# Kernel tuning notes

Hardware: AMD Instinct MI355X
Metric: run time of the kernel (lower is better)

## Reference

```python
import jax, jax.numpy as jnp
import numpy as np

N = 50000
E = 800000
IN_C = 128
HID = 64
HEADS = 4
OUT_C = 64
NEG_SLOPE = 0.2


def gat_conv(x, edge_index, W, att_src, att_dst, bias, heads, out_ch, concat):
    """PyG-style GATConv (add_self_loops=True, eval mode: no dropout)."""
    n = x.shape[0]
    loop = jnp.arange(n, dtype=edge_index.dtype)
    src = jnp.concatenate([edge_index[0], loop])
    dst = jnp.concatenate([edge_index[1], loop])
    h = (x @ W).reshape(n, heads, out_ch)              # [N,H,C]
    a_s = jnp.einsum('nhc,hc->nh', h, att_src)          # [N,H]
    a_d = jnp.einsum('nhc,hc->nh', h, att_dst)
    e = jax.nn.leaky_relu(a_s[src] + a_d[dst], NEG_SLOPE)  # [E',H]
    m = jax.ops.segment_max(e, dst, num_segments=n)
    m = jnp.where(jnp.isfinite(m), m, 0.0)
    ex = jnp.exp(e - m[dst])
    denom = jax.ops.segment_sum(ex, dst, num_segments=n)
    alpha = ex / (denom[dst] + 1e-16)                   # segment softmax over incoming edges
    out = jax.ops.segment_sum(alpha[:, :, None] * h[src], dst, num_segments=n)  # [N,H,C]
    out = out.reshape(n, heads * out_ch) if concat else out.mean(axis=1)
    return out + bias


def setup_inputs() -> dict:
    key = jax.random.key(0)
    ks = jax.random.split(key, 20)
    s = 0.1
    inp = {
        'x': jax.random.normal(ks[0], (N, IN_C), dtype=jnp.float32),
        'pos_edge_index': jax.random.randint(ks[1], (2, E), 0, N, dtype=jnp.int32),
        'neg_edge_index': jax.random.randint(ks[2], (2, E), 0, N, dtype=jnp.int32),
        # layer 0 pos
        'W0p': jax.random.normal(ks[3], (IN_C, HEADS * HID), jnp.float32) * s,
        'asrc0p': jax.random.normal(ks[4], (HEADS, HID), jnp.float32) * s,
        'adst0p': jax.random.normal(ks[5], (HEADS, HID), jnp.float32) * s,
        'b0p': jnp.zeros((HEADS * HID,), jnp.float32),
        # layer 0 neg
        'W0n': jax.random.normal(ks[6], (IN_C, HEADS * HID), jnp.float32) * s,
        'asrc0n': jax.random.normal(ks[7], (HEADS, HID), jnp.float32) * s,
        'adst0n': jax.random.normal(ks[8], (HEADS, HID), jnp.float32) * s,
        'b0n': jnp.zeros((HEADS * HID,), jnp.float32),
        # layer 1 pos (heads=1, concat=False)
        'W1p': jax.random.normal(ks[9], (HEADS * HID, OUT_C), jnp.float32) * s,
        'asrc1p': jax.random.normal(ks[10], (1, OUT_C), jnp.float32) * s,
        'adst1p': jax.random.normal(ks[11], (1, OUT_C), jnp.float32) * s,
        'b1p': jnp.zeros((OUT_C,), jnp.float32),
        # layer 1 neg
        'W1n': jax.random.normal(ks[12], (HEADS * HID, OUT_C), jnp.float32) * s,
        'asrc1n': jax.random.normal(ks[13], (1, OUT_C), jnp.float32) * s,
        'adst1n': jax.random.normal(ks[14], (1, OUT_C), jnp.float32) * s,
        'b1n': jnp.zeros((OUT_C,), jnp.float32),
    }
    return inp


def reference(x, pos_edge_index, neg_edge_index,
              W0p, asrc0p, adst0p, b0p,
              W0n, asrc0n, adst0n, b0n,
              W1p, asrc1p, adst1p, b1p,
              W1n, asrc1n, adst1n, b1n):
    xp = gat_conv(x, pos_edge_index, W0p, asrc0p, adst0p, b0p, HEADS, HID, True)
    xn = gat_conv(x, neg_edge_index, W0n, asrc0n, adst0n, b0n, HEADS, HID, True)
    h = jax.nn.elu(xp - xn)  # dropout is identity in eval mode
    op = gat_conv(h, pos_edge_index, W1p, asrc1p, adst1p, b1p, 1, OUT_C, False)
    on = gat_conv(h, neg_edge_index, W1n, asrc1n, adst1n, b1n, 1, OUT_C, False)
    return op - on
```

## Files before the change

### kernel.cpp

```cpp
#include <hip/hip_runtime.h>
#include <cstdint>

#define N_NODES 50000
#define N_EDGES 800000

typedef __attribute__((ext_vector_type(8))) short bf16x8;
typedef __attribute__((ext_vector_type(4))) float f32x4;

__device__ __forceinline__ float lrelu(float x) { return x >= 0.f ? x : 0.2f * x; }

__device__ __forceinline__ void onup(float& m, float& s, float e) {
  float nm = fmaxf(m, e);
  s = s * __expf(m - nm) + __expf(e - nm);
  m = nm;
}

__device__ __forceinline__ unsigned short f2b(float f) {
  unsigned int u = __float_as_uint(f);
  u += 0x7FFFu + ((u >> 16) & 1u);
  return (unsigned short)(u >> 16);
}
__device__ __forceinline__ float blo(unsigned int u) { return __uint_as_float(u << 16); }
__device__ __forceinline__ float bhi(unsigned int u) { return __uint_as_float(u & 0xFFFF0000u); }

__device__ __forceinline__ float sel4(float v0, float v1, float v2, float v3, int h) {
  float r = v0;
  r = (h == 1) ? v1 : r;
  r = (h == 2) ? v2 : r;
  r = (h == 3) ? v3 : r;
  return r;
}


__global__ __launch_bounds__(256) void k_hist2(const int* __restrict__ ep, const int* __restrict__ en,
                                               int* __restrict__ cntP, int* __restrict__ cntN, int E, int half) {
  int b = blockIdx.x;
  const int* ei = (b < half) ? ep : en;
  int* cnt = (b < half) ? cntP : cntN;
  int e = (b % half) * 256 + threadIdx.x;
  if (e < E) atomicAdd(&cnt[ei[E + e]], 1);
}

__global__ __launch_bounds__(256) void k_scan_partial2(const int* __restrict__ cntP, const int* __restrict__ cntN,
                                                       int* __restrict__ partP, int* __restrict__ partN,
                                                       int N, int half) {
  int b = blockIdx.x;
  const int* cnt = (b < half) ? cntP : cntN;
  int* partial = (b < half) ? partP : partN;
  int bb = b % half;
  int t = threadIdx.x;
  int sum = 0;
#pragma unroll
  for (int i = 0; i < 4; i++) {
    int idx = bb * 1024 + i * 256 + t;
    if (idx < N) sum += cnt[idx];
  }
#pragma unroll
  for (int o = 32; o; o >>= 1) sum += __shfl_xor(sum, o);
  __shared__ int sh[4];
  if ((t & 63) == 0) sh[t >> 6] = sum;
  __syncthreads();
  if (t == 0) partial[bb] = sh[0] + sh[1] + sh[2] + sh[3];
}

__global__ __launch_bounds__(64) void k_scan_top2(const int* __restrict__ partP, const int* __restrict__ partN,
                                                  int* __restrict__ prefP, int* __restrict__ prefN,
                                                  int nb, int* __restrict__ offPN, int* __restrict__ offNN, int total) {
  const int* partial = (blockIdx.x == 0) ? partP : partN;
  int* pref = (blockIdx.x == 0) ? prefP : prefN;
  int* offN = (blockIdx.x == 0) ? offPN : offNN;
  int l = threadIdx.x;
  int v = (l < nb) ? partial[l] : 0;
  int x = v;
#pragma unroll
  for (int o = 1; o < 64; o <<= 1) {
    int y = __shfl_up(x, o);
    if (l >= o) x += y;
  }
  if (l < nb) pref[l] = x - v;
  if (l == 0) *offN = total;
}

__global__ __launch_bounds__(256) void k_scan_final2(const int* __restrict__ cntP, const int* __restrict__ cntN,
                                                     const int* __restrict__ prefP, const int* __restrict__ prefN,
                                                     int* __restrict__ offP, int* __restrict__ offN,
                                                     int N, int half) {
  int b = blockIdx.x;
  const int* cnt = (b < half) ? cntP : cntN;
  const int* pref = (b < half) ? prefP : prefN;
  int* off = (b < half) ? offP : offN;
  int bb = b % half;
  int t = threadIdx.x;
  int idx0 = bb * 1024 + t * 4;
  int v0 = (idx0 + 0 < N) ? cnt[idx0 + 0] : 0;
  int v1 = (idx0 + 1 < N) ? cnt[idx0 + 1] : 0;
  int v2 = (idx0 + 2 < N) ? cnt[idx0 + 2] : 0;
  int v3 = (idx0 + 3 < N) ? cnt[idx0 + 3] : 0;
  int s = v0 + v1 + v2 + v3;
  int lane = t & 63, w = t >> 6;
  int x = s;
#pragma unroll
  for (int o = 1; o < 64; o <<= 1) {
    int y = __shfl_up(x, o);
    if (lane >= o) x += y;
  }
  __shared__ int wtot[4];
  if (lane == 63) wtot[w] = x;
  __syncthreads();
  int woff = 0;
#pragma unroll
  for (int i = 0; i < 4; i++)
    if (i < w) woff += wtot[i];
  int excl = pref[bb] + woff + (x - s);
  if (idx0 + 0 < N) off[idx0 + 0] = excl;
  excl += v0;
  if (idx0 + 1 < N) off[idx0 + 1] = excl;
  excl += v1;
  if (idx0 + 2 < N) off[idx0 + 2] = excl;
  excl += v2;
  if (idx0 + 3 < N) off[idx0 + 3] = excl;
}

__global__ __launch_bounds__(256) void k_scatter2(const int* __restrict__ ep, const int* __restrict__ en,
                                                  const int* __restrict__ offP, const int* __restrict__ offN,
                                                  int* __restrict__ cntP, int* __restrict__ cntN,
                                                  int* __restrict__ srtP, int* __restrict__ srtN, int E, int half) {
  int b = blockIdx.x;
  const int* ei = (b < half) ? ep : en;
  const int* off = (b < half) ? offP : offN;
  int* cnt = (b < half) ? cntP : cntN;
  int* srt = (b < half) ? srtP : srtN;
  int e = (b % half) * 256 + threadIdx.x;
  if (e < E) {
    int s = ei[e], d = ei[E + e];
    int p = atomicSub(&cnt[d], 1) - 1;
    srt[off[d] + p] = s;
  }
}


__global__ __launch_bounds__(256) void k_prep(const float* __restrict__ x,
                                              const float* __restrict__ W0p, const float* __restrict__ W0n,
                                              const float* __restrict__ W1p, const float* __restrict__ W1n,
                                              unsigned short* __restrict__ xb,
                                              unsigned short* __restrict__ w0f,
                                              unsigned short* __restrict__ w1f) {
  int b = blockIdx.x, t = threadIdx.x;
  if (b < 3125) {
    int base = (b * 256 + t) * 8;
    float4 v0 = *(const float4*)&x[base];
    float4 v1 = *(const float4*)&x[base + 4];
    ushort4 a, c;
    a.x = f2b(v0.x); a.y = f2b(v0.y); a.z = f2b(v0.z); a.w = f2b(v0.w);
    c.x = f2b(v1.x); c.y = f2b(v1.y); c.z = f2b(v1.z); c.w = f2b(v1.w);
    *(ushort4*)&xb[base] = a;
    *(ushort4*)&xb[base + 4] = c;
  } else if (b < 3157) {
    int tid = (b - 3125) * 256 + t;
    int lane = tid & 63;
    int rest = tid >> 6;
    int ks = rest & 3; rest >>= 2;
    int n = rest & 3;
    int g = rest >> 2;
    int col = (g & 3) * 64 + n * 16 + (lane & 15);
    const float* W = (g < 4) ? W0p : W0n;
    size_t dst = ((((size_t)(g * 4 + n)) * 4 + ks) * 64 + lane) * 8;
#pragma unroll
    for (int j = 0; j < 8; j++) {
      int k = ks * 32 + (lane >> 4) * 8 + j;
      w0f[dst + j] = f2b(W[k * 256 + col]);
    }
  } else {
    int tid = (b - 3157) * 256 + t;
    int lane = tid & 63;
    int rest = tid >> 6;
    int ks = rest & 7; rest >>= 3;
    int n = rest & 3;
    int g = rest >> 2;
    int col = n * 16 + (lane & 15);
    const float* W = g ? W1n : W1p;
    size_t dst = ((((size_t)(g * 4 + n)) * 8 + ks) * 64 + lane) * 8;
#pragma unroll
    for (int j = 0; j < 8; j++) {
      int k = ks * 32 + (lane >> 4) * 8 + j;
      w1f[dst + j] = f2b(W[k * 64 + col]);
    }
  }
}


template <int KSTEPS, int CBF16, int H, int NC>
__global__ __launch_bounds__(256) void k_mgemm(const unsigned short* __restrict__ Ab,
                                               const unsigned short* __restrict__ Bf,
                                               unsigned short* __restrict__ Cb, float* __restrict__ Cf,
                                               int Nrows,
                                               const float* __restrict__ attSP, const float* __restrict__ attDP,
                                               const float* __restrict__ attSN, const float* __restrict__ attDN,
                                               float* __restrict__ oSP, float* __restrict__ oDP,
                                               float* __restrict__ oSN, float* __restrict__ oDN) {
  constexpr int K = KSTEPS * 32;
  int wm = threadIdx.x >> 6, lane = threadIdx.x & 63;
  int row0 = blockIdx.x * 128 + wm * 32;
  int g = blockIdx.y;
  const bf16x8* Bv = (const bf16x8*)Bf;
  const bf16x8* Av = (const bf16x8*)Ab;

  f32x4 acc[2][4];
#pragma unroll
  for (int mi = 0; mi < 2; mi++)
#pragma unroll
    for (int n = 0; n < 4; n++) acc[mi][n] = (f32x4){0.f, 0.f, 0.f, 0.f};

  int r0 = row0 + (lane & 15);
  int r1 = r0 + 16;
  bool v0 = r0 < Nrows, v1 = r1 < Nrows;
  size_t arow0 = (size_t)r0 * (K / 8) + (lane >> 4);
  size_t arow1 = (size_t)r1 * (K / 8) + (lane >> 4);
  const bf16x8 az = {0, 0, 0, 0, 0, 0, 0, 0};

  for (int kh = 0; kh < KSTEPS / 4; kh++) {
#pragma unroll
    for (int k4 = 0; k4 < 4; k4++) {
      int ks = kh * 4 + k4;
      bf16x8 a0 = v0 ? Av[arow0 + ks * 4] : az;
      bf16x8 a1 = v1 ? Av[arow1 + ks * 4] : az;
      bf16x8 b0 = Bv[((size_t)(g * 4 + 0) * KSTEPS + ks) * 64 + lane];
      bf16x8 b1 = Bv[((size_t)(g * 4 + 1) * KSTEPS + ks) * 64 + lane];
      bf16x8 b2 = Bv[((size_t)(g * 4 + 2) * KSTEPS + ks) * 64 + lane];
      bf16x8 b3 = Bv[((size_t)(g * 4 + 3) * KSTEPS + ks) * 64 + lane];
      acc[0][0] = __builtin_amdgcn_mfma_f32_16x16x32_bf16(a0, b0, acc[0][0], 0, 0, 0);
      acc[0][1] = __builtin_amdgcn_mfma_f32_16x16x32_bf16(a0, b1, acc[0][1], 0, 0, 0);
      acc[0][2] = __builtin_amdgcn_mfma_f32_16x16x32_bf16(a0, b2, acc[0][2], 0, 0, 0);
      acc[0][3] = __builtin_amdgcn_mfma_f32_16x16x32_bf16(a0, b3, acc[0][3], 0, 0, 0);
      acc[1][0] = __builtin_amdgcn_mfma_f32_16x16x32_bf16(a1, b0, acc[1][0], 0, 0, 0);
      acc[1][1] = __builtin_amdgcn_mfma_f32_16x16x32_bf16(a1, b1, acc[1][1], 0, 0, 0);
      acc[1][2] = __builtin_amdgcn_mfma_f32_16x16x32_bf16(a1, b2, acc[1][2], 0, 0, 0);
      acc[1][3] = __builtin_amdgcn_mfma_f32_16x16x32_bf16(a1, b3, acc[1][3], 0, 0, 0);
    }
  }

#pragma unroll
  for (int mi = 0; mi < 2; mi++)
#pragma unroll
    for (int n = 0; n < 4; n++)
#pragma unroll
      for (int reg = 0; reg < 4; reg++) {
        int row = row0 + mi * 16 + (lane >> 4) * 4 + reg;
        int col = g * 64 + n * 16 + (lane & 15);
        if (row < Nrows) {
          if (CBF16)
            Cb[(size_t)row * NC + col] = f2b(acc[mi][n][reg]);
          else
            Cf[(size_t)row * NC + col] = acc[mi][n][reg];
        }
      }

  constexpr int POSG = NC / 128;
  int isNeg = (g >= POSG) ? 1 : 0;
  int head = isNeg ? g - POSG : g;
  const float* wS = (isNeg ? attSN : attSP) + head * 64;
  const float* wD = (isNeg ? attDN : attDP) + head * 64;
  float* oS = isNeg ? oSN : oSP;
  float* oD = isNeg ? oDN : oDP;
  float ws0 = wS[0 * 16 + (lane & 15)], ws1 = wS[1 * 16 + (lane & 15)];
  float ws2 = wS[2 * 16 + (lane & 15)], ws3 = wS[3 * 16 + (lane & 15)];
  float wd0 = wD[0 * 16 + (lane & 15)], wd1 = wD[1 * 16 + (lane & 15)];
  float wd2 = wD[2 * 16 + (lane & 15)], wd3 = wD[3 * 16 + (lane & 15)];
#pragma unroll
  for (int mi = 0; mi < 2; mi++)
#pragma unroll
    for (int reg = 0; reg < 4; reg++) {
      float ps = acc[mi][0][reg] * ws0 + acc[mi][1][reg] * ws1 + acc[mi][2][reg] * ws2 + acc[mi][3][reg] * ws3;
      float pd = acc[mi][0][reg] * wd0 + acc[mi][1][reg] * wd1 + acc[mi][2][reg] * wd2 + acc[mi][3][reg] * wd3;
#pragma unroll
      for (int o = 1; o < 16; o <<= 1) {
        ps += __shfl_xor(ps, o);
        pd += __shfl_xor(pd, o);
      }
      int row = row0 + mi * 16 + (lane >> 4) * 4 + reg;
      if ((lane & 15) == 0 && row < Nrows) {
        oS[(size_t)row * H + head] = ps;
        oD[(size_t)row * H + head] = pd;
      }
    }
}


struct MS4 { float m0, m1, m2, m3, s0, s1, s2, s3; };

__device__ __forceinline__ MS4 stats_heads(const float* __restrict__ as, float4 sl, float4 ad,
                                           const int* __restrict__ srt, int base, int deg, int l) {
  MS4 r;
  r.m0 = r.m1 = r.m2 = r.m3 = -1e30f;
  r.s0 = r.s1 = r.s2 = r.s3 = 0.f;
  if (l == 0) {
    r.m0 = lrelu(sl.x + ad.x); r.s0 = 1.f;
    r.m1 = lrelu(sl.y + ad.y); r.s1 = 1.f;
    r.m2 = lrelu(sl.z + ad.z); r.s2 = 1.f;
    r.m3 = lrelu(sl.w + ad.w); r.s3 = 1.f;
  }
  for (int i = l; i < deg; i += 64) {
    int s = srt[base + i];
    float4 av = *(const float4*)&as[(size_t)s * 4];
    onup(r.m0, r.s0, lrelu(av.x + ad.x));
    onup(r.m1, r.s1, lrelu(av.y + ad.y));
    onup(r.m2, r.s2, lrelu(av.z + ad.z));
    onup(r.m3, r.s3, lrelu(av.w + ad.w));
  }
#pragma unroll
  for (int o = 32; o; o >>= 1) {
    float mo, so, nm;
    mo = __shfl_xor(r.m0, o); so = __shfl_xor(r.s0, o);
    nm = fmaxf(r.m0, mo); r.s0 = r.s0 * __expf(r.m0 - nm) + so * __expf(mo - nm); r.m0 = nm;
    mo = __shfl_xor(r.m1, o); so = __shfl_xor(r.s1, o);
    nm = fmaxf(r.m1, mo); r.s1 = r.s1 * __expf(r.m1 - nm) + so * __expf(mo - nm); r.m1 = nm;
    mo = __shfl_xor(r.m2, o); so = __shfl_xor(r.s2, o);
    nm = fmaxf(r.m2, mo); r.s2 = r.s2 * __expf(r.m2 - nm) + so * __expf(mo - nm); r.m2 = nm;
    mo = __shfl_xor(r.m3, o); so = __shfl_xor(r.s3, o);
    nm = fmaxf(r.m3, mo); r.s3 = r.s3 * __expf(r.m3 - nm) + so * __expf(mo - nm); r.m3 = nm;
  }
  return r;
}


__device__ __forceinline__ float4 gather0b(const unsigned short* __restrict__ h0b, int colElem,
                                           const float* __restrict__ as, int hl, float adh,
                                           float mh, float inv, float wself, int n,
                                           const int* __restrict__ srt, int base, int deg, int l) {
  float4 acc;
  {
    uint2 hv = *(const uint2*)&h0b[(size_t)n * 512 + colElem];
    acc.x = wself * blo(hv.x); acc.y = wself * bhi(hv.x);
    acc.z = wself * blo(hv.y); acc.w = wself * bhi(hv.y);
  }
  for (int j = 0; j < deg; j += 8) {
    int idx[8];
    float w[8];
#pragma unroll
    for (int s2 = 0; s2 < 8; s2++) {
      int jj = j + s2;
      bool v = jj < deg;
      int p = base + (v ? jj : 0);
      int si = srt[p];
      idx[s2] = si;
      float e = lrelu(as[(size_t)si * 4 + hl] + adh);
      w[s2] = v ? __expf(e - mh) * inv : 0.f;
    }
#pragma unroll
    for (int s2 = 0; s2 < 8; s2++) {
      uint2 hv = *(const uint2*)&h0b[(size_t)idx[s2] * 512 + colElem];
      acc.x = fmaf(w[s2], blo(hv.x), acc.x);
      acc.y = fmaf(w[s2], bhi(hv.x), acc.y);
      acc.z = fmaf(w[s2], blo(hv.y), acc.z);
      acc.w = fmaf(w[s2], bhi(hv.y), acc.w);
    }
  }
  return acc;
}

__global__ __launch_bounds__(256) void k_agg0f(const unsigned short* __restrict__ h0b,
                                               const float* __restrict__ asP, const float* __restrict__ adP,
                                               const float* __restrict__ asN, const float* __restrict__ adN,
                                               const int* __restrict__ offP, const int* __restrict__ srtP,
                                               const int* __restrict__ offN, const int* __restrict__ srtN,
                                               const float* __restrict__ bP, const float* __restrict__ bN,
                                               unsigned short* __restrict__ xb, int N) {
  int n = blockIdx.x * 4 + (threadIdx.x >> 6);
  if (n >= N) return;
  int l = threadIdx.x & 63;
  int hl = l >> 4;

  int baseP = offP[n], degP = offP[n + 1] - baseP;
  float4 adp4 = *(const float4*)&adP[(size_t)n * 4];
  float4 asp4 = *(const float4*)&asP[(size_t)n * 4];
  MS4 P = stats_heads(asP, asp4, adp4, srtP, baseP, degP, l);
  float mhP = sel4(P.m0, P.m1, P.m2, P.m3, hl);
  float invP = 1.f / (sel4(P.s0, P.s1, P.s2, P.s3, hl) + 1e-16f);
  float adhP = sel4(adp4.x, adp4.y, adp4.z, adp4.w, hl);
  float ashP = sel4(asp4.x, asp4.y, asp4.z, asp4.w, hl);
  float wselfP = __expf(lrelu(ashP + adhP) - mhP) * invP;
  float4 accP = gather0b(h0b, l * 4, asP, hl, adhP, mhP, invP, wselfP, n, srtP, baseP, degP, l);

  int baseN = offN[n], degN = offN[n + 1] - baseN;
  float4 adn4 = *(const float4*)&adN[(size_t)n * 4];
  float4 asn4 = *(const float4*)&asN[(size_t)n * 4];
  MS4 Q = stats_heads(asN, asn4, adn4, srtN, baseN, degN, l);
  float mhN = sel4(Q.m0, Q.m1, Q.m2, Q.m3, hl);
  float invN = 1.f / (sel4(Q.s0, Q.s1, Q.s2, Q.s3, hl) + 1e-16f);
  float adhN = sel4(adn4.x, adn4.y, adn4.z, adn4.w, hl);
  float ashN = sel4(asn4.x, asn4.y, asn4.z, asn4.w, hl);
  float wselfN = __expf(lrelu(ashN + adhN) - mhN) * invN;
  float4 accN = gather0b(h0b, 256 + l * 4, asN, hl, adhN, mhN, invN, wselfN, n, srtN, baseN, degN, l);

  float4 bp = *(const float4*)&bP[l * 4];
  float4 bn = *(const float4*)&bN[l * 4];
  float rx = accP.x + bp.x - accN.x - bn.x;
  float ry = accP.y + bp.y - accN.y - bn.y;
  float rz = accP.z + bp.z - accN.z - bn.z;
  float rw = accP.w + bp.w - accN.w - bn.w;
  rx = rx > 0.f ? rx : expm1f(rx);
  ry = ry > 0.f ? ry : expm1f(ry);
  rz = rz > 0.f ? rz : expm1f(rz);
  rw = rw > 0.f ? rw : expm1f(rw);
  ushort4 r;
  r.x = f2b(rx); r.y = f2b(ry); r.z = f2b(rz); r.w = f2b(rw);
  *(ushort4*)&xb[(size_t)n * 256 + l * 4] = r;
}


__device__ __forceinline__ void stats1(const float* __restrict__ as, float sl, float ad,
                                       const int* __restrict__ srt, int base, int deg, int l,
                                       float& m, float& s) {
  m = -1e30f;
  s = 0.f;
  if (l == 0) {
    m = lrelu(sl + ad);
    s = 1.f;
  }
  for (int i = l; i < deg; i += 64) onup(m, s, lrelu(as[srt[base + i]] + ad));
#pragma unroll
  for (int o = 32; o; o >>= 1) {
    float mo = __shfl_xor(m, o);
    float so = __shfl_xor(s, o);
    float nm = fmaxf(m, mo);
    s = s * __expf(m - nm) + so * __expf(mo - nm);
    m = nm;
  }
}

__device__ __forceinline__ float gather1_half(const float* __restrict__ h1, int colOff,
                                              const float* __restrict__ as, float ad, float mh, float inv,
                                              float wself, int n, const int* __restrict__ srt, int base, int deg,
                                              int l) {
  float acc = wself * h1[(size_t)n * 128 + colOff + l];
  for (int j = 0; j < deg; j += 8) {
    int idx[8];
    float w[8];
#pragma unroll
    for (int s2 = 0; s2 < 8; s2++) {
      int jj = j + s2;
      bool v = jj < deg;
      int p = base + (v ? jj : 0);
      int si = srt[p];
      idx[s2] = si;
      w[s2] = v ? __expf(lrelu(as[si] + ad) - mh) * inv : 0.f;
    }
#pragma unroll
    for (int s2 = 0; s2 < 8; s2++) acc = fmaf(w[s2], h1[(size_t)idx[s2] * 128 + colOff + l], acc);
  }
  return acc;
}

__global__ __launch_bounds__(256) void k_agg1f(const float* __restrict__ h1,
                                               const float* __restrict__ asP, const float* __restrict__ adP,
                                               const float* __restrict__ asN, const float* __restrict__ adN,
                                               const int* __restrict__ offP, const int* __restrict__ srtP,
                                               const int* __restrict__ offN, const int* __restrict__ srtN,
                                               const float* __restrict__ bP, const float* __restrict__ bN,
                                               float* __restrict__ out, int N) {
  int n = blockIdx.x * 4 + (threadIdx.x >> 6);
  if (n >= N) return;
  int l = threadIdx.x & 63;

  int baseP = offP[n], degP = offP[n + 1] - baseP;
  float adp = adP[n], asp = asP[n];
  float mP, sP;
  stats1(asP, asp, adp, srtP, baseP, degP, l, mP, sP);
  float invP = 1.f / (sP + 1e-16f);
  float wselfP = __expf(lrelu(asp + adp) - mP) * invP;
  float accP = gather1_half(h1, 0, asP, adp, mP, invP, wselfP, n, srtP, baseP, degP, l);

  int baseN = offN[n], degN = offN[n + 1] - baseN;
  float adn = adN[n], asn = asN[n];
  float mN, sN;
  stats1(asN, asn, adn, srtN, baseN, degN, l, mN, sN);
  float invN = 1.f / (sN + 1e-16f);
  float wselfN = __expf(lrelu(asn + adn) - mN) * invN;
  float accN = gather1_half(h1, 64, asN, adn, mN, invN, wselfN, n, srtN, baseN, degN, l);

  out[(size_t)n * 64 + l] = (accP + bP[l]) - (accN + bN[l]);
}


extern "C" void kernel_launch(void* const* d_in, const int* in_sizes, int n_in,
                              void* d_out, int out_size, void* d_ws, size_t ws_size,
                              hipStream_t stream) {
  const float* x = (const float*)d_in[0];
  const int* ep = (const int*)d_in[1];
  const int* en = (const int*)d_in[2];
  const float* W0p = (const float*)d_in[3];
  const float* asrc0p = (const float*)d_in[4];
  const float* adst0p = (const float*)d_in[5];
  const float* b0p = (const float*)d_in[6];
  const float* W0n = (const float*)d_in[7];
  const float* asrc0n = (const float*)d_in[8];
  const float* adst0n = (const float*)d_in[9];
  const float* b0n = (const float*)d_in[10];
  const float* W1p = (const float*)d_in[11];
  const float* asrc1p = (const float*)d_in[12];
  const float* adst1p = (const float*)d_in[13];
  const float* b1p = (const float*)d_in[14];
  const float* W1n = (const float*)d_in[15];
  const float* asrc1n = (const float*)d_in[16];
  const float* adst1n = (const float*)d_in[17];
  const float* b1n = (const float*)d_in[18];

  const int N = N_NODES, E = N_EDGES;
  char* base = (char*)d_ws;
  size_t o = 0;
  auto alloc = [&](size_t bytes) -> void* {
    void* r = base + o;
    o = (o + bytes + 255) & ~(size_t)255;
    return r;
  };
  int* cnt_p = (int*)alloc((size_t)N * 4);
  int* cnt_n = (int*)alloc((size_t)N * 4);
  size_t cntBytes = o;
  int* off_p = (int*)alloc((size_t)(N + 1) * 4);
  int* off_n = (int*)alloc((size_t)(N + 1) * 4);
  int* part_p = (int*)alloc(1024 * 4);
  int* part_n = (int*)alloc(1024 * 4);
  int* pref_p = (int*)alloc(1024 * 4);
  int* pref_n = (int*)alloc(1024 * 4);
  int* srt_p = (int*)alloc((size_t)E * 4);
  int* srt_n = (int*)alloc((size_t)E * 4);
  unsigned short* xb16 = (unsigned short*)alloc((size_t)N * 128 * 2);
  unsigned short* w0f = (unsigned short*)alloc(65536 * 2);
  unsigned short* w1f = (unsigned short*)alloc(32768 * 2);
  unsigned short* h0b = (unsigned short*)alloc((size_t)N * 512 * 2);
  float* as0p = (float*)alloc((size_t)N * 4 * 4);
  float* ad0p = (float*)alloc((size_t)N * 4 * 4);
  float* as0n = (float*)alloc((size_t)N * 4 * 4);
  float* ad0n = (float*)alloc((size_t)N * 4 * 4);
  float* as1p = (float*)alloc((size_t)N * 4);
  float* ad1p = (float*)alloc((size_t)N * 4);
  float* as1n = (float*)alloc((size_t)N * 4);
  float* ad1n = (float*)alloc((size_t)N * 4);
  unsigned short* xbufb = (unsigned short*)alloc((size_t)N * 256 * 2);
  float* h1 = (float*)alloc((size_t)N * 128 * 4);

  hipMemsetAsync(base, 0, cntBytes, stream);

  int egrid = (E + 255) / 256;
  int nb = (N + 1023) / 1024;
  k_hist2<<<2 * egrid, 256, 0, stream>>>(ep, en, cnt_p, cnt_n, E, egrid);
  k_scan_partial2<<<2 * nb, 256, 0, stream>>>(cnt_p, cnt_n, part_p, part_n, N, nb);
  k_scan_top2<<<2, 64, 0, stream>>>(part_p, part_n, pref_p, pref_n, nb, off_p + N, off_n + N, E);
  k_scan_final2<<<2 * nb, 256, 0, stream>>>(cnt_p, cnt_n, pref_p, pref_n, off_p, off_n, N, nb);
  k_scatter2<<<2 * egrid, 256, 0, stream>>>(ep, en, off_p, off_n, cnt_p, cnt_n, srt_p, srt_n, E, egrid);

  k_prep<<<3173, 256, 0, stream>>>(x, W0p, W0n, W1p, W1n, xb16, w0f, w1f);

  int ngrid = (N + 3) / 4;
  int mgrid = (N + 127) / 128;

  dim3 g0(mgrid, 8);
  k_mgemm<4, 1, 4, 512><<<g0, 256, 0, stream>>>(xb16, w0f, h0b, (float*)nullptr, N,
                                                asrc0p, adst0p, asrc0n, adst0n,
                                                as0p, ad0p, as0n, ad0n);
  k_agg0f<<<ngrid, 256, 0, stream>>>(h0b, as0p, ad0p, as0n, ad0n,
                                     off_p, srt_p, off_n, srt_n, b0p, b0n, xbufb, N);

  dim3 g1(mgrid, 2);
  k_mgemm<8, 0, 1, 128><<<g1, 256, 0, stream>>>(xbufb, w1f, (unsigned short*)nullptr, h1, N,
                                                asrc1p, adst1p, asrc1n, adst1n,
                                                as1p, ad1p, as1n, ad1n);
  k_agg1f<<<ngrid, 256, 0, stream>>>(h1, as1p, ad1p, as1n, ad1n,
                                     off_p, srt_p, off_n, srt_n, b1p, b1n, (float*)d_out, N);
}
```

Measured before the change: 637.8 us.

## Split attention softmax into separate per-edge exp pass and gather pass

Replaces the fused online-softmax stats plus gather with a separate kernel that computes exp(leaky_relu(e)) per edge without max subtraction, stores it into per-edge alpha buffers, and writes per-node inverse sums and self-loop weights. The gather kernels then read the precomputed alpha and scale by the inverse sum at the end. This avoids recomputing exps and the online max/rescale in the gather. In exchange it adds kernel launches and writes and reads of per-edge alpha arrays. Dropping the max subtraction risks overflow for large logits.

```diff
diff --git a/kernel.cpp b/kernel.cpp
--- a/kernel.cpp
+++ b/kernel.cpp
@@ -8,12 +8,6 @@
 typedef __attribute__((ext_vector_type(4))) float f32x4;
 
 __device__ __forceinline__ float lrelu(float x) { return x >= 0.f ? x : 0.2f * x; }
-
-__device__ __forceinline__ void onup(float& m, float& s, float e) {
-  float nm = fmaxf(m, e);
-  s = s * __expf(m - nm) + __expf(e - nm);
-  m = nm;
-}
 
 __device__ __forceinline__ unsigned short f2b(float f) {
   unsigned int u = __float_as_uint(f);
@@ -22,14 +16,6 @@
 }
 __device__ __forceinline__ float blo(unsigned int u) { return __uint_as_float(u << 16); }
 __device__ __forceinline__ float bhi(unsigned int u) { return __uint_as_float(u & 0xFFFF0000u); }
-
-__device__ __forceinline__ float sel4(float v0, float v1, float v2, float v3, int h) {
-  float r = v0;
-  r = (h == 1) ? v1 : r;
-  r = (h == 2) ? v2 : r;
-  r = (h == 3) ? v3 : r;
-  return r;
-}
 
 
 __global__ __launch_bounds__(256) void k_hist2(const int* __restrict__ ep, const int* __restrict__ en,
@@ -286,53 +272,96 @@
 }
 
 
-struct MS4 { float m0, m1, m2, m3, s0, s1, s2, s3; };
-
-__device__ __forceinline__ MS4 stats_heads(const float* __restrict__ as, float4 sl, float4 ad,
-                                           const int* __restrict__ srt, int base, int deg, int l) {
-  MS4 r;
-  r.m0 = r.m1 = r.m2 = r.m3 = -1e30f;
-  r.s0 = r.s1 = r.s2 = r.s3 = 0.f;
-  if (l == 0) {
-    r.m0 = lrelu(sl.x + ad.x); r.s0 = 1.f;
-    r.m1 = lrelu(sl.y + ad.y); r.s1 = 1.f;
-    r.m2 = lrelu(sl.z + ad.z); r.s2 = 1.f;
-    r.m3 = lrelu(sl.w + ad.w); r.s3 = 1.f;
-  }
-  for (int i = l; i < deg; i += 64) {
-    int s = srt[base + i];
-    float4 av = *(const float4*)&as[(size_t)s * 4];
-    onup(r.m0, r.s0, lrelu(av.x + ad.x));
-    onup(r.m1, r.s1, lrelu(av.y + ad.y));
-    onup(r.m2, r.s2, lrelu(av.z + ad.z));
-    onup(r.m3, r.s3, lrelu(av.w + ad.w));
-  }
-#pragma unroll
-  for (int o = 32; o; o >>= 1) {
-    float mo, so, nm;
-    mo = __shfl_xor(r.m0, o); so = __shfl_xor(r.s0, o);
-    nm = fmaxf(r.m0, mo); r.s0 = r.s0 * __expf(r.m0 - nm) + so * __expf(mo - nm); r.m0 = nm;
-    mo = __shfl_xor(r.m1, o); so = __shfl_xor(r.s1, o);
-    nm = fmaxf(r.m1, mo); r.s1 = r.s1 * __expf(r.m1 - nm) + so * __expf(mo - nm); r.m1 = nm;
-    mo = __shfl_xor(r.m2, o); so = __shfl_xor(r.s2, o);
-    nm = fmaxf(r.m2, mo); r.s2 = r.s2 * __expf(r.m2 - nm) + so * __expf(mo - nm); r.m2 = nm;
-    mo = __shfl_xor(r.m3, o); so = __shfl_xor(r.s3, o);
-    nm = fmaxf(r.m3, mo); r.s3 = r.s3 * __expf(r.m3 - nm) + so * __expf(mo - nm); r.m3 = nm;
-  }
-  return r;
+__global__ __launch_bounds__(256) void k_sa0(const float* __restrict__ asP, const float* __restrict__ adP,
+                                             const int* __restrict__ offP, const int* __restrict__ srtP,
+                                             float* __restrict__ alphaP, float* __restrict__ invP,
+                                             float* __restrict__ wslfP,
+                                             const float* __restrict__ asN, const float* __restrict__ adN,
+                                             const int* __restrict__ offN, const int* __restrict__ srtN,
+                                             float* __restrict__ alphaN, float* __restrict__ invN,
+                                             float* __restrict__ wslfN, int N) {
+  int n = blockIdx.x * 4 + (threadIdx.x >> 6);
+  if (n >= N) return;
+  int l = threadIdx.x & 63;
+  {
+    int base = offP[n], deg = offP[n + 1] - base;
+    float4 ad4 = *(const float4*)&adP[(size_t)n * 4];
+    float s0 = 0.f, s1 = 0.f, s2 = 0.f, s3 = 0.f;
+    for (int i = l; i < deg; i += 64) {
+      int s = srtP[base + i];
+      float4 av = *(const float4*)&asP[(size_t)s * 4];
+      float4 ex;
+      ex.x = __expf(lrelu(av.x + ad4.x));
+      ex.y = __expf(lrelu(av.y + ad4.y));
+      ex.z = __expf(lrelu(av.z + ad4.z));
+      ex.w = __expf(lrelu(av.w + ad4.w));
+      *(float4*)&alphaP[(size_t)(base + i) * 4] = ex;
+      s0 += ex.x; s1 += ex.y; s2 += ex.z; s3 += ex.w;
+    }
+#pragma unroll
+    for (int o = 32; o; o >>= 1) {
+      s0 += __shfl_xor(s0, o);
+      s1 += __shfl_xor(s1, o);
+      s2 += __shfl_xor(s2, o);
+      s3 += __shfl_xor(s3, o);
+    }
+    if (l == 0) {
+      float4 as4 = *(const float4*)&asP[(size_t)n * 4];
+      float e0 = __expf(lrelu(as4.x + ad4.x));
+      float e1 = __expf(lrelu(as4.y + ad4.y));
+      float e2 = __expf(lrelu(as4.z + ad4.z));
+      float e3 = __expf(lrelu(as4.w + ad4.w));
+      float i0 = 1.f / (s0 + e0 + 1e-16f);
+      float i1 = 1.f / (s1 + e1 + 1e-16f);
+      float i2 = 1.f / (s2 + e2 + 1e-16f);
+      float i3 = 1.f / (s3 + e3 + 1e-16f);
+      *(float4*)&invP[(size_t)n * 4] = make_float4(i0, i1, i2, i3);
+      *(float4*)&wslfP[(size_t)n * 4] = make_float4(e0 * i0, e1 * i1, e2 * i2, e3 * i3);
+    }
+  }
+  {
+    int base = offN[n], deg = offN[n + 1] - base;
+    float4 ad4 = *(const float4*)&adN[(size_t)n * 4];
+    float s0 = 0.f, s1 = 0.f, s2 = 0.f, s3 = 0.f;
+    for (int i = l; i < deg; i += 64) {
+      int s = srtN[base + i];
+      float4 av = *(const float4*)&asN[(size_t)s * 4];
+      float4 ex;
+      ex.x = __expf(lrelu(av.x + ad4.x));
+      ex.y = __expf(lrelu(av.y + ad4.y));
+      ex.z = __expf(lrelu(av.z + ad4.z));
+      ex.w = __expf(lrelu(av.w + ad4.w));
+      *(float4*)&alphaN[(size_t)(base + i) * 4] = ex;
+      s0 += ex.x; s1 += ex.y; s2 += ex.z; s3 += ex.w;
+    }
+#pragma unroll
+    for (int o = 32; o; o >>= 1) {
+      s0 += __shfl_xor(s0, o);
+      s1 += __shfl_xor(s1, o);
+      s2 += __shfl_xor(s2, o);
+      s3 += __shfl_xor(s3, o);
+    }
+    if (l == 0) {
+      float4 as4 = *(const float4*)&asN[(size_t)n * 4];
+      float e0 = __expf(lrelu(as4.x + ad4.x));
+      float e1 = __expf(lrelu(as4.y + ad4.y));
+      float e2 = __expf(lrelu(as4.z + ad4.z));
+      float e3 = __expf(lrelu(as4.w + ad4.w));
+      float i0 = 1.f / (s0 + e0 + 1e-16f);
+      float i1 = 1.f / (s1 + e1 + 1e-16f);
+      float i2 = 1.f / (s2 + e2 + 1e-16f);
+      float i3 = 1.f / (s3 + e3 + 1e-16f);
+      *(float4*)&invN[(size_t)n * 4] = make_float4(i0, i1, i2, i3);
+      *(float4*)&wslfN[(size_t)n * 4] = make_float4(e0 * i0, e1 * i1, e2 * i2, e3 * i3);
+    }
+  }
 }
 
 
 __device__ __forceinline__ float4 gather0b(const unsigned short* __restrict__ h0b, int colElem,
-                                           const float* __restrict__ as, int hl, float adh,
-                                           float mh, float inv, float wself, int n,
-                                           const int* __restrict__ srt, int base, int deg, int l) {
-  float4 acc;
-  {
-    uint2 hv = *(const uint2*)&h0b[(size_t)n * 512 + colElem];
-    acc.x = wself * blo(hv.x); acc.y = wself * bhi(hv.x);
-    acc.z = wself * blo(hv.y); acc.w = wself * bhi(hv.y);
-  }
+                                           const float* __restrict__ alpha, int hl,
+                                           const int* __restrict__ srt, int base, int deg) {
+  float4 acc = make_float4(0.f, 0.f, 0.f, 0.f);
   for (int j = 0; j < deg; j += 8) {
     int idx[8];
     float w[8];
@@ -341,10 +370,8 @@
       int jj = j + s2;
       bool v = jj < deg;
       int p = base + (v ? jj : 0);
-      int si = srt[p];
-      idx[s2] = si;
-      float e = lrelu(as[(size_t)si * 4 + hl] + adh);
-      w[s2] = v ? __expf(e - mh) * inv : 0.f;
+      idx[s2] = srt[p];
+      w[s2] = v ? alpha[(size_t)p * 4 + hl] : 0.f;
     }
 #pragma unroll
     for (int s2 = 0; s2 < 8; s2++) {
@@ -358,39 +385,43 @@
   return acc;
 }
 
-__global__ __launch_bounds__(256) void k_agg0f(const unsigned short* __restrict__ h0b,
-                                               const float* __restrict__ asP, const float* __restrict__ adP,
-                                               const float* __restrict__ asN, const float* __restrict__ adN,
-                                               const int* __restrict__ offP, const int* __restrict__ srtP,
-                                               const int* __restrict__ offN, const int* __restrict__ srtN,
-                                               const float* __restrict__ bP, const float* __restrict__ bN,
-                                               unsigned short* __restrict__ xb, int N) {
+__global__ __launch_bounds__(256) void k_gather0(const unsigned short* __restrict__ h0b,
+                                                 const int* __restrict__ offP, const int* __restrict__ srtP,
+                                                 const float* __restrict__ alphaP, const float* __restrict__ invP,
+                                                 const float* __restrict__ wslfP,
+                                                 const int* __restrict__ offN, const int* __restrict__ srtN,
+                                                 const float* __restrict__ alphaN, const float* __restrict__ invN,
+                                                 const float* __restrict__ wslfN,
+                                                 const float* __restrict__ bP, const float* __restrict__ bN,
+                                                 unsigned short* __restrict__ xb, int N) {
   int n = blockIdx.x * 4 + (threadIdx.x >> 6);
   if (n >= N) return;
   int l = threadIdx.x & 63;
   int hl = l >> 4;
 
   int baseP = offP[n], degP = offP[n + 1] - baseP;
-  float4 adp4 = *(const float4*)&adP[(size_t)n * 4];
-  float4 asp4 = *(const float4*)&asP[(size_t)n * 4];
-  MS4 P = stats_heads(asP, asp4, adp4, srtP, baseP, degP, l);
-  float mhP = sel4(P.m0, P.m1, P.m2, P.m3, hl);
-  float invP = 1.f / (sel4(P.s0, P.s1, P.s2, P.s3, hl) + 1e-16f);
-  float adhP = sel4(adp4.x, adp4.y, adp4.z, adp4.w, hl);
-  float ashP = sel4(asp4.x, asp4.y, asp4.z, asp4.w, hl);
-  float wselfP = __expf(lrelu(ashP + adhP) - mhP) * invP;
-  float4 accP = gather0b(h0b, l * 4, asP, hl, adhP, mhP, invP, wselfP, n, srtP, baseP, degP, l);
+  float4 accP = gather0b(h0b, l * 4, alphaP, hl, srtP, baseP, degP);
+  {
+    float iv = invP[(size_t)n * 4 + hl];
+    float ws = wslfP[(size_t)n * 4 + hl];
+    uint2 hs = *(const uint2*)&h0b[(size_t)n * 512 + l * 4];
+    accP.x = fmaf(accP.x, iv, ws * blo(hs.x));
+    accP.y = fmaf(accP.y, iv, ws * bhi(hs.x));
+    accP.z = fmaf(accP.z, iv, ws * blo(hs.y));
+    accP.w = fmaf(accP.w, iv, ws * bhi(hs.y));
+  }
 
   int baseN = offN[n], degN = offN[n + 1] - baseN;
-  float4 adn4 = *(const float4*)&adN[(size_t)n * 4];
-  float4 asn4 = *(const float4*)&asN[(size_t)n * 4];
-  MS4 Q = stats_heads(asN, asn4, adn4, srtN, baseN, degN, l);
-  float mhN = sel4(Q.m0, Q.m1, Q.m2, Q.m3, hl);
-  float invN = 1.f / (sel4(Q.s0, Q.s1, Q.s2, Q.s3, hl) + 1e-16f);
-  float adhN = sel4(adn4.x, adn4.y, adn4.z, adn4.w, hl);
-  float ashN = sel4(asn4.x, asn4.y, asn4.z, asn4.w, hl);
-  float wselfN = __expf(lrelu(ashN + adhN) - mhN) * invN;
-  float4 accN = gather0b(h0b, 256 + l * 4, asN, hl, adhN, mhN, invN, wselfN, n, srtN, baseN, degN, l);
+  float4 accN = gather0b(h0b, 256 + l * 4, alphaN, hl, srtN, baseN, degN);
+  {
+    float iv = invN[(size_t)n * 4 + hl];
+    float ws = wslfN[(size_t)n * 4 + hl];
+    uint2 hs = *(const uint2*)&h0b[(size_t)n * 512 + 256 + l * 4];
+    accN.x = fmaf(accN.x, iv, ws * blo(hs.x));
+    accN.y = fmaf(accN.y, iv, ws * bhi(hs.x));
+    accN.z = fmaf(accN.z, iv, ws * blo(hs.y));
+    accN.w = fmaf(accN.w, iv, ws * bhi(hs.y));
+  }
 
   float4 bp = *(const float4*)&bP[l * 4];
   float4 bn = *(const float4*)&bN[l * 4];
@@ -408,31 +439,59 @@
 }
 
 
-__device__ __forceinline__ void stats1(const float* __restrict__ as, float sl, float ad,
-                                       const int* __restrict__ srt, int base, int deg, int l,
-                                       float& m, float& s) {
-  m = -1e30f;
-  s = 0.f;
-  if (l == 0) {
-    m = lrelu(sl + ad);
-    s = 1.f;
-  }
-  for (int i = l; i < deg; i += 64) onup(m, s, lrelu(as[srt[base + i]] + ad));
-#pragma unroll
-  for (int o = 32; o; o >>= 1) {
-    float mo = __shfl_xor(m, o);
-    float so = __shfl_xor(s, o);
-    float nm = fmaxf(m, mo);
-    s = s * __expf(m - nm) + so * __expf(mo - nm);
-    m = nm;
-  }
-}
-
-__device__ __forceinline__ float gather1_half(const float* __restrict__ h1, int colOff,
-                                              const float* __restrict__ as, float ad, float mh, float inv,
-                                              float wself, int n, const int* __restrict__ srt, int base, int deg,
-                                              int l) {
-  float acc = wself * h1[(size_t)n * 128 + colOff + l];
+__global__ __launch_bounds__(256) void k_sa1(const float* __restrict__ asP, const float* __restrict__ adP,
+                                             const int* __restrict__ offP, const int* __restrict__ srtP,
+                                             float* __restrict__ alphaP, float* __restrict__ invP,
+                                             float* __restrict__ wslfP,
+                                             const float* __restrict__ asN, const float* __restrict__ adN,
+                                             const int* __restrict__ offN, const int* __restrict__ srtN,
+                                             float* __restrict__ alphaN, float* __restrict__ invN,
+                                             float* __restrict__ wslfN, int N) {
+  int n = blockIdx.x * 4 + (threadIdx.x >> 6);
+  if (n >= N) return;
+  int l = threadIdx.x & 63;
+  {
+    int base = offP[n], deg = offP[n + 1] - base;
+    float ad = adP[n];
+    float s = 0.f;
+    for (int i = l; i < deg; i += 64) {
+      float ex = __expf(lrelu(asP[srtP[base + i]] + ad));
+      alphaP[base + i] = ex;
+      s += ex;
+    }
+#pragma unroll
+    for (int o = 32; o; o >>= 1) s += __shfl_xor(s, o);
+    if (l == 0) {
+      float se = __expf(lrelu(asP[n] + ad));
+      float iv = 1.f / (s + se + 1e-16f);
+      invP[n] = iv;
+      wslfP[n] = se * iv;
+    }
+  }
+  {
+    int base = offN[n], deg = offN[n + 1] - base;
+    float ad = adN[n];
+    float s = 0.f;
+    for (int i = l; i < deg; i += 64) {
+      float ex = __expf(lrelu(asN[srtN[base + i]] + ad));
+      alphaN[base + i] = ex;
+      s += ex;
+    }
+#pragma unroll
+    for (int o = 32; o; o >>= 1) s += __shfl_xor(s, o);
+    if (l == 0) {
+      float se = __expf(lrelu(asN[n] + ad));
+      float iv = 1.f / (s + se + 1e-16f);
+      invN[n] = iv;
+      wslfN[n] = se * iv;
+    }
+  }
+}
+
+__device__ __forceinline__ float gather1b(const float* __restrict__ h1, int colIdx,
+                                          const float* __restrict__ alpha,
+                                          const int* __restrict__ srt, int base, int deg) {
+  float acc = 0.f;
   for (int j = 0; j < deg; j += 8) {
     int idx[8];
     float w[8];
@@ -441,42 +500,35 @@
       int jj = j + s2;
       bool v = jj < deg;
       int p = base + (v ? jj : 0);
-      int si = srt[p];
-      idx[s2] = si;
-      w[s2] = v ? __expf(lrelu(as[si] + ad) - mh) * inv : 0.f;
-    }
-#pragma unroll
-    for (int s2 = 0; s2 < 8; s2++) acc = fmaf(w[s2], h1[(size_t)idx[s2] * 128 + colOff + l], acc);
+      idx[s2] = srt[p];
+      w[s2] = v ? alpha[p] : 0.f;
+    }
+#pragma unroll
+    for (int s2 = 0; s2 < 8; s2++) acc = fmaf(w[s2], h1[(size_t)idx[s2] * 128 + colIdx], acc);
   }
   return acc;
 }
 
-__global__ __launch_bounds__(256) void k_agg1f(const float* __restrict__ h1,
-                                               const float* __restrict__ asP, const float* __restrict__ adP,
-                                               const float* __restrict__ asN, const float* __restrict__ adN,
-                                               const int* __restrict__ offP, const int* __restrict__ srtP,
-                                               const int* __restrict__ offN, const int* __restrict__ srtN,
-                                               const float* __restrict__ bP, const float* __restrict__ bN,
-                                               float* __restrict__ out, int N) {
+__global__ __launch_bounds__(256) void k_gather1(const float* __restrict__ h1,
+                                                 const int* __restrict__ offP, const int* __restrict__ srtP,
+                                                 const float* __restrict__ alphaP, const float* __restrict__ invP,
+                                                 const float* __restrict__ wslfP,
+                                                 const int* __restrict__ offN, const int* __restrict__ srtN,
+                                                 const float* __restrict__ alphaN, const float* __restrict__ invN,
+                                                 const float* __restrict__ wslfN,
+                                                 const float* __restrict__ bP, const float* __restrict__ bN,
+                                                 float* __restrict__ out, int N) {
   int n = blockIdx.x * 4 + (threadIdx.x >> 6);
   if (n >= N) return;
   int l = threadIdx.x & 63;
 
   int baseP = offP[n], degP = offP[n + 1] - baseP;
-  float adp = adP[n], asp = asP[n];
-  float mP, sP;
-  stats1(asP, asp, adp, srtP, baseP, degP, l, mP, sP);
-  float invP = 1.f / (sP + 1e-16f);
-  float wselfP = __expf(lrelu(asp + adp) - mP) * invP;
-  float accP = gather1_half(h1, 0, asP, adp, mP, invP, wselfP, n, srtP, baseP, degP, l);
+  float accP = gather1b(h1, l, alphaP, srtP, baseP, degP);
+  accP = fmaf(accP, invP[n], wslfP[n] * h1[(size_t)n * 128 + l]);
 
   int baseN = offN[n], degN = offN[n + 1] - baseN;
-  float adn = adN[n], asn = asN[n];
-  float mN, sN;
-  stats1(asN, asn, adn, srtN, baseN, degN, l, mN, sN);
-  float invN = 1.f / (sN + 1e-16f);
-  float wselfN = __expf(lrelu(asn + adn) - mN) * invN;
-  float accN = gather1_half(h1, 64, asN, adn, mN, invN, wselfN, n, srtN, baseN, degN, l);
+  float accN = gather1b(h1, 64 + l, alphaN, srtN, baseN, degN);
+  accN = fmaf(accN, invN[n], wslfN[n] * h1[(size_t)n * 128 + 64 + l]);
 
   out[(size_t)n * 64 + l] = (accP + bP[l]) - (accN + bN[l]);
 }
@@ -536,6 +588,18 @@
   float* ad1p = (float*)alloc((size_t)N * 4);
   float* as1n = (float*)alloc((size_t)N * 4);
   float* ad1n = (float*)alloc((size_t)N * 4);
+  float* inv0p = (float*)alloc((size_t)N * 4 * 4);
+  float* wslf0p = (float*)alloc((size_t)N * 4 * 4);
+  float* inv0n = (float*)alloc((size_t)N * 4 * 4);
+  float* wslf0n = (float*)alloc((size_t)N * 4 * 4);
+  float* inv1p = (float*)alloc((size_t)N * 4);
+  float* wslf1p = (float*)alloc((size_t)N * 4);
+  float* inv1n = (float*)alloc((size_t)N * 4);
+  float* wslf1n = (float*)alloc((size_t)N * 4);
+  float* alpha0p = (float*)alloc((size_t)E * 4 * 4);
+  float* alpha0n = (float*)alloc((size_t)E * 4 * 4);
+  float* alpha1p = (float*)alloc((size_t)E * 4);
+  float* alpha1n = (float*)alloc((size_t)E * 4);
   unsigned short* xbufb = (unsigned short*)alloc((size_t)N * 256 * 2);
   float* h1 = (float*)alloc((size_t)N * 128 * 4);
 
@@ -558,13 +622,17 @@
   k_mgemm<4, 1, 4, 512><<<g0, 256, 0, stream>>>(xb16, w0f, h0b, (float*)nullptr, N,
                                                 asrc0p, adst0p, asrc0n, adst0n,
                                                 as0p, ad0p, as0n, ad0n);
-  k_agg0f<<<ngrid, 256, 0, stream>>>(h0b, as0p, ad0p, as0n, ad0n,
-                                     off_p, srt_p, off_n, srt_n, b0p, b0n, xbufb, N);
+  k_sa0<<<ngrid, 256, 0, stream>>>(as0p, ad0p, off_p, srt_p, alpha0p, inv0p, wslf0p,
+                                   as0n, ad0n, off_n, srt_n, alpha0n, inv0n, wslf0n, N);
+  k_gather0<<<ngrid, 256, 0, stream>>>(h0b, off_p, srt_p, alpha0p, inv0p, wslf0p,
+                                       off_n, srt_n, alpha0n, inv0n, wslf0n, b0p, b0n, xbufb, N);
 
   dim3 g1(mgrid, 2);
   k_mgemm<8, 0, 1, 128><<<g1, 256, 0, stream>>>(xbufb, w1f, (unsigned short*)nullptr, h1, N,
                                                 asrc1p, adst1p, asrc1n, adst1n,
                                                 as1p, ad1p, as1n, ad1n);
-  k_agg1f<<<ngrid, 256, 0, stream>>>(h1, as1p, ad1p, as1n, ad1n,
-                                     off_p, srt_p, off_n, srt_n, b1p, b1n, (float*)d_out, N);
-}
+  k_sa1<<<ngrid, 256, 0, stream>>>(as1p, ad1p, off_p, srt_p, alpha1p, inv1p, wslf1p,
+                                   as1n, ad1n, off_n, srt_n, alpha1n, inv1n, wslf1n, N);
+  k_gather1<<<ngrid, 256, 0, stream>>>(h1, off_p, srt_p, alpha1p, inv1p, wslf1p,
+                                       off_n, srt_n, alpha1n, inv1n, wslf1n, b1p, b1n, (float*)d_out, N);
+}
```

Measured after the change: 577.7 us. 1.1x faster.
